# Optimization experiments

Measured on AMD Instinct MI355X. Metric: run time of the kernel, lower is better.

The kernel has to match this reference:

```python
import jax, jax.numpy as jnp
import numpy as np

N_NODES = 50000
NODE_DIM = 128
HIDDEN = 128
N_EDGES = 1600000
N_POSTS = 8192


def setup_inputs() -> dict:
    key = jax.random.key(0)
    ks = jax.random.split(key, 12)
    glorot = lambda k, shp: jax.random.normal(k, shp, jnp.float32) * (1.0 / np.sqrt(shp[0]))
    inp = {
        "node_features": jax.random.normal(ks[0], (N_NODES, NODE_DIM), jnp.float32),
        "edge_index": jax.random.randint(ks[1], (2, N_EDGES), 0, N_NODES, jnp.int32),
        "post_mask": jax.random.randint(ks[2], (N_POSTS,), 0, N_NODES, jnp.int32),
        # node_encoder: node_dim -> hidden
        "W_enc": glorot(ks[3], (NODE_DIM, HIDDEN)),
        "b_enc": jnp.zeros((HIDDEN,), jnp.float32),
        # conv1/conv2: hidden -> hidden
        "W1": glorot(ks[4], (HIDDEN, HIDDEN)),
        "b1": jnp.zeros((HIDDEN,), jnp.float32),
        "W2": glorot(ks[5], (HIDDEN, HIDDEN)),
        "b2": jnp.zeros((HIDDEN,), jnp.float32),
        # output head: hidden -> hidden//2 -> 1
        "W_o1": glorot(ks[6], (HIDDEN, HIDDEN // 2)),
        "b_o1": jnp.zeros((HIDDEN // 2,), jnp.float32),
        "W_o2": glorot(ks[7], (HIDDEN // 2, 1)),
        "b_o2": jnp.zeros((1,), jnp.float32),
    }
    return inp


def _aggregate(h, src, dst, n_nodes):
    # sum_{e: dst[e]=v} h[src[e]]  -- vectorized scatter-add (segment_sum)
    return jax.ops.segment_sum(h[src], dst, num_segments=n_nodes)


def reference(node_features, edge_index, post_mask,
              W_enc, b_enc, W1, b1, W2, b2, W_o1, b_o1, W_o2, b_o2):
    src, dst = edge_index[0], edge_index[1]
    n = node_features.shape[0]

    h = jax.nn.relu(node_features @ W_enc + b_enc)          # [N, H]
    agg = _aggregate(h, src, dst, n)                        # [N, H]
    h = jax.nn.relu((agg + h) @ W1 + b1)
    agg = _aggregate(h, src, dst, n)
    h = jax.nn.relu((agg + h) @ W2 + b2)

    post = h[post_mask]                                     # [P, H]
    hid = jax.nn.relu(post @ W_o1 + b_o1)                   # [P, H//2]
    logits = (hid @ W_o2 + b_o2).squeeze(-1)                # [P]
    return jax.nn.sigmoid(logits)
```

## Files before the change

kernel.cpp:

```cpp
#include <hip/hip_runtime.h>
#include <math.h>


typedef unsigned long long u64;

#define RB_SIZE   4096
#define RB_ROUNDS 16

__global__ __launch_bounds__(1024) void scan_part(const int* __restrict__ in,
                                                  int* __restrict__ bsum, int n) {
    __shared__ int red[1024];
    int i = blockIdx.x * 1024 + threadIdx.x;
    red[threadIdx.x] = (i < n) ? in[i] : 0;
    __syncthreads();
    for (int d = 512; d; d >>= 1) {
        if (threadIdx.x < d) red[threadIdx.x] += red[threadIdx.x + d];
        __syncthreads();
    }
    if (threadIdx.x == 0) bsum[blockIdx.x] = red[0];
}

__global__ __launch_bounds__(256) void scan_tops_par(const int* __restrict__ bsum,
                                                     int* __restrict__ bbase, int nb) {
    __shared__ int buf[256];
    int tid = threadIdx.x;
    int v = (tid < nb) ? bsum[tid] : 0;
    buf[tid] = v;
    __syncthreads();
    for (int s = 1; s < 256; s <<= 1) {
        int u = (tid >= s) ? buf[tid - s] : 0;
        __syncthreads();
        buf[tid] += u;
        __syncthreads();
    }
    if (tid < nb) bbase[tid] = buf[tid] - v;
}

__global__ __launch_bounds__(1024) void scan_final(const int* __restrict__ in,
                                                   const int* __restrict__ bbase,
                                                   int* __restrict__ out, int n) {
    __shared__ int buf[1024];
    int tid = threadIdx.x;
    int i = blockIdx.x * 1024 + tid;
    int c = (i < n) ? in[i] : 0;
    buf[tid] = c;
    __syncthreads();
    for (int d = 1; d < 1024; d <<= 1) {
        int v = (tid >= d) ? buf[tid - d] : 0;
        __syncthreads();
        buf[tid] += v;
        __syncthreads();
    }
    if (i < n) out[i] = bbase[blockIdx.x] + buf[tid] - c;
}

template <bool FIRST>
__global__ __launch_bounds__(256) void radix_hist(const int* __restrict__ dstArr,
                                                  const u64* __restrict__ recIn,
                                                  int* __restrict__ blockhist,
                                                  int E, int NBLK) {
    __shared__ int cnt[256];
    cnt[threadIdx.x] = 0;
    __syncthreads();
    int base = blockIdx.x * RB_SIZE;
    for (int t = threadIdx.x; t < RB_SIZE; t += 256) {
        int i = base + t;
        if (i < E) {
            int d = FIRST ? (dstArr[i] & 255)
                          : (int)((recIn[i] >> 8) & 255);
            atomicAdd(&cnt[d], 1);
        }
    }
    __syncthreads();
    blockhist[threadIdx.x * NBLK + blockIdx.x] = cnt[threadIdx.x];
}

template <bool FIRST>
__global__ __launch_bounds__(256) void radix_scatter(const int* __restrict__ dstArr,
                                                     const int* __restrict__ srcArr,
                                                     const u64* __restrict__ recIn,
                                                     u64* __restrict__ recOut,
                                                     int* __restrict__ csr_src,
                                                     int* __restrict__ csr_dst,
                                                     const int* __restrict__ blockbase,
                                                     int E, int NBLK) {
    __shared__ int cursor[256];
    __shared__ int gbase[256];
    __shared__ int cnt[256 * 4];
    __shared__ int wbase[256 * 4];
    int tid = threadIdx.x;
    int wid = tid >> 6, lane = tid & 63;
    cursor[tid] = 0;
    gbase[tid] = blockbase[tid * NBLK + blockIdx.x];
    int base = blockIdx.x * RB_SIZE;
    __syncthreads();
    for (int r = 0; r < RB_ROUNDS; ++r) {
        int i = base + r * 256 + tid;
        bool valid = (i < E);
        int d = 0;
        u64 rec = 0;
        if (valid) {
            if (FIRST) {
                int dv = dstArr[i];
                rec = ((u64)(unsigned)srcArr[i] << 32) | (unsigned)dv;
                d = dv & 255;
            } else {
                rec = recIn[i];
                d = (int)((rec >> 8) & 255);
            }
        }
        ((int4*)cnt)[tid] = make_int4(0, 0, 0, 0);
        u64 mask = ~0ull;
#pragma unroll
        for (int b = 0; b < 8; ++b) {
            int bit = (d >> b) & 1;
            u64 bal = __ballot(bit);
            mask &= bit ? bal : ~bal;
        }
        mask &= __ballot(valid ? 1 : 0);
        int rank = __popcll(mask & (((u64)1 << lane) - 1));
        int wtot = __popcll(mask);
        __syncthreads();
        if (valid && rank == 0) cnt[d * 4 + wid] = wtot;
        __syncthreads();
        {
            int run = cursor[tid];
#pragma unroll
            for (int w = 0; w < 4; ++w) {
                wbase[tid * 4 + w] = run;
                run += cnt[tid * 4 + w];
            }
            cursor[tid] = run;
        }
        __syncthreads();
        if (valid) {
            int pos = gbase[d] + wbase[d * 4 + wid] + rank;
            if (FIRST) {
                recOut[pos] = rec;
            } else {
                csr_src[pos] = (int)(rec >> 32);
                csr_dst[pos] = (int)(rec & 0xffffffffu);
            }
        }
        __syncthreads();
    }
}

__global__ __launch_bounds__(256) void boundary_kernel(const int* __restrict__ csr_dst,
                                                       int* __restrict__ offs,
                                                       int E, int N) {
    int e = blockIdx.x * 256 + threadIdx.x;
    if (e >= E) return;
    int cur = csr_dst[e];
    int prev = (e == 0) ? -1 : csr_dst[e - 1];
    for (int v = prev + 1; v <= cur; ++v) offs[v] = e;
    if (e == E - 1)
        for (int v = cur + 1; v <= N; ++v) offs[v] = E;
}

template <bool FUSE>
__global__ __launch_bounds__(256) void gemm128(const float* __restrict__ A,
                                               const float* __restrict__ A2,
                                               const float* __restrict__ W,
                                               const float* __restrict__ bias,
                                               float* __restrict__ out, int M) {
    __shared__ float Ws[64 * 128];
    __shared__ float As[32 * 128];
    int tid = threadIdx.x;
    int row0 = blockIdx.x * 32;

    float4* As4 = (float4*)As;
#pragma unroll
    for (int i = 0; i < 4; ++i) {
        int idx = tid + 256 * i;
        int r = idx >> 5, c = idx & 31;
        int gr = row0 + r;
        float4 v = make_float4(0.f, 0.f, 0.f, 0.f);
        if (gr < M) {
            v = ((const float4*)A)[gr * 32 + c];
            if (FUSE) {
                float4 u = ((const float4*)A2)[gr * 32 + c];
                v.x += u.x; v.y += u.y; v.z += u.z; v.w += u.w;
            }
        }
        As4[idx] = v;
    }

    int tx = tid & 31, ty = tid >> 5;
    float acc[4][4];
#pragma unroll
    for (int r = 0; r < 4; ++r)
#pragma unroll
        for (int c = 0; c < 4; ++c) acc[r][c] = 0.f;

    const float4* W4 = (const float4*)W;
    float4* Ws4 = (float4*)Ws;

    for (int kh = 0; kh < 2; ++kh) {
        __syncthreads();
#pragma unroll
        for (int i = 0; i < 8; ++i)
            Ws4[tid + 256 * i] = W4[kh * 2048 + tid + 256 * i];
        __syncthreads();

#pragma unroll 2
        for (int k = 0; k < 64; k += 4) {
            float4 a[4], b[4];
#pragma unroll
            for (int r = 0; r < 4; ++r)
                a[r] = *(const float4*)&As[(ty * 4 + r) * 128 + kh * 64 + k];
#pragma unroll
            for (int kk = 0; kk < 4; ++kk)
                b[kk] = *(const float4*)&Ws[(k + kk) * 128 + tx * 4];
#pragma unroll
            for (int r = 0; r < 4; ++r) {
                acc[r][0] = fmaf(a[r].x, b[0].x, acc[r][0]);
                acc[r][1] = fmaf(a[r].x, b[0].y, acc[r][1]);
                acc[r][2] = fmaf(a[r].x, b[0].z, acc[r][2]);
                acc[r][3] = fmaf(a[r].x, b[0].w, acc[r][3]);
                acc[r][0] = fmaf(a[r].y, b[1].x, acc[r][0]);
                acc[r][1] = fmaf(a[r].y, b[1].y, acc[r][1]);
                acc[r][2] = fmaf(a[r].y, b[1].z, acc[r][2]);
                acc[r][3] = fmaf(a[r].y, b[1].w, acc[r][3]);
                acc[r][0] = fmaf(a[r].z, b[2].x, acc[r][0]);
                acc[r][1] = fmaf(a[r].z, b[2].y, acc[r][1]);
                acc[r][2] = fmaf(a[r].z, b[2].z, acc[r][2]);
                acc[r][3] = fmaf(a[r].z, b[2].w, acc[r][3]);
                acc[r][0] = fmaf(a[r].w, b[3].x, acc[r][0]);
                acc[r][1] = fmaf(a[r].w, b[3].y, acc[r][1]);
                acc[r][2] = fmaf(a[r].w, b[3].z, acc[r][2]);
                acc[r][3] = fmaf(a[r].w, b[3].w, acc[r][3]);
            }
        }
    }

    float4 bv = *(const float4*)&bias[tx * 4];
#pragma unroll
    for (int r = 0; r < 4; ++r) {
        int gr = row0 + ty * 4 + r;
        if (gr < M) {
            float4 o;
            o.x = fmaxf(acc[r][0] + bv.x, 0.f);
            o.y = fmaxf(acc[r][1] + bv.y, 0.f);
            o.z = fmaxf(acc[r][2] + bv.z, 0.f);
            o.w = fmaxf(acc[r][3] + bv.w, 0.f);
            ((float4*)out)[gr * 32 + tx] = o;
        }
    }
}

__global__ __launch_bounds__(256) void aggregate_kernel(const float* __restrict__ h,
                                                        const int* __restrict__ offs,
                                                        const int* __restrict__ csr_src,
                                                        float* __restrict__ agg, int n) {
    int w = (blockIdx.x * 256 + threadIdx.x) >> 6;
    int lane = threadIdx.x & 63;
    int half = lane >> 5;
    int l32 = lane & 31;
    int node = w * 2 + half;
    bool nvalid = node < n;
    int beg = 0, deg = 0;
    if (nvalid) {
        beg = offs[node];
        deg = offs[node + 1] - beg;
    }
    int mdeg = max(deg, __shfl_xor(deg, 32));
    const float4* h4 = (const float4*)h;
    float ax = 0.f, ay = 0.f, az = 0.f, aw = 0.f;
    for (int base = 0; base < mdeg; base += 32) {
        int idx = base + l32;
        int sv = (nvalid && idx < deg) ? csr_src[beg + idx] : 0;
        int nk = mdeg - base; if (nk > 32) nk = 32;
#pragma unroll 4
        for (int j = 0; j < nk; ++j) {
            int s = __shfl(sv, (half << 5) | j);
            if (base + j < deg) {
                float4 r = h4[s * 32 + l32];
                ax += r.x; ay += r.y; az += r.z; aw += r.w;
            }
        }
    }
    if (nvalid) {
        float4 o = make_float4(ax, ay, az, aw);
        ((float4*)agg)[(size_t)node * 32 + l32] = o;
    }
}

__global__ __launch_bounds__(256) void head_kernel(const float* __restrict__ h,
                                                   const int* __restrict__ mask,
                                                   const float* __restrict__ Wo1,
                                                   const float* __restrict__ bo1,
                                                   const float* __restrict__ Wo2,
                                                   const float* __restrict__ bo2,
                                                   float* __restrict__ out, int P) {
    __shared__ float hids[4][64];
    int wid = threadIdx.x >> 6;
    int lane = threadIdx.x & 63;
    int p = blockIdx.x * 4 + wid;
    if (p >= P) return;
    int node = mask[p];
    const float* row = h + (size_t)node * 128;
    float acc = 0.f;
#pragma unroll 4
    for (int k = 0; k < 128; ++k)
        acc = fmaf(row[k], Wo1[k * 64 + lane], acc);
    hids[wid][lane] = fmaxf(acc + bo1[lane], 0.f);
    if (lane == 0) {
        double lg = 0.0;
        for (int j = 0; j < 64; ++j)
            lg = fma((double)hids[wid][j], (double)Wo2[j], lg);
        lg += (double)bo2[0];
        out[p] = (float)(1.0 / (1.0 + exp(-lg)));
    }
}

extern "C" void kernel_launch(void* const* d_in, const int* in_sizes, int n_in,
                              void* d_out, int out_size, void* d_ws, size_t ws_size,
                              hipStream_t stream) {
    const float* NF   = (const float*)d_in[0];
    const int*   EI   = (const int*)d_in[1];
    const int*   MASK = (const int*)d_in[2];
    const float* Wenc = (const float*)d_in[3];
    const float* benc = (const float*)d_in[4];
    const float* W1   = (const float*)d_in[5];
    const float* b1   = (const float*)d_in[6];
    const float* W2   = (const float*)d_in[7];
    const float* b2   = (const float*)d_in[8];
    const float* Wo1  = (const float*)d_in[9];
    const float* bo1  = (const float*)d_in[10];
    const float* Wo2  = (const float*)d_in[11];
    const float* bo2  = (const float*)d_in[12];
    float* out = (float*)d_out;

    const int N = in_sizes[0] / 128;
    const int E = in_sizes[1] / 2;
    const int P = in_sizes[2];

    char* ws = (char*)d_ws;
    size_t off = 0;
    auto alloc = [&](size_t bytes) {
        char* pp = ws + off;
        off += (bytes + 255) & ~(size_t)255;
        return pp;
    };
    float* h       = (float*)alloc((size_t)N * 128 * 4);
    float* agg     = (float*)alloc((size_t)N * 128 * 4);
    int*   offs    = (int*)alloc((size_t)(N + 1) * 4);
    int*   csr_src = (int*)alloc((size_t)E * 4);
    const int NBLK = (E + RB_SIZE - 1) / RB_SIZE;
    int*   bh      = (int*)alloc((size_t)256 * NBLK * 4);
    int*   bb      = (int*)alloc((size_t)256 * NBLK * 4);
    int*   bsum    = (int*)alloc(256 * 4);
    int*   bbase   = (int*)alloc(256 * 4);
    u64* rec_a   = (u64*)h;
    int* csr_dst = (int*)agg;

    const int* src = EI;
    const int* dst = EI + E;

    const int L = 256 * NBLK;
    const int nscanL = (L + 1023) / 1024;
    radix_hist<true><<<NBLK, 256, 0, stream>>>(dst, nullptr, bh, E, NBLK);
    scan_part<<<nscanL, 1024, 0, stream>>>(bh, bsum, L);
    scan_tops_par<<<1, 256, 0, stream>>>(bsum, bbase, nscanL);
    scan_final<<<nscanL, 1024, 0, stream>>>(bh, bbase, bb, L);
    radix_scatter<true><<<NBLK, 256, 0, stream>>>(dst, src, nullptr, rec_a,
                                                  nullptr, nullptr, bb, E, NBLK);
    radix_hist<false><<<NBLK, 256, 0, stream>>>(nullptr, rec_a, bh, E, NBLK);
    scan_part<<<nscanL, 1024, 0, stream>>>(bh, bsum, L);
    scan_tops_par<<<1, 256, 0, stream>>>(bsum, bbase, nscanL);
    scan_final<<<nscanL, 1024, 0, stream>>>(bh, bbase, bb, L);
    radix_scatter<false><<<NBLK, 256, 0, stream>>>(nullptr, nullptr, rec_a, nullptr,
                                                   csr_src, csr_dst, bb, E, NBLK);

    boundary_kernel<<<(E + 255) / 256, 256, 0, stream>>>(csr_dst, offs, E, N);

    int gblocks = (N + 31) / 32;
    int ablocks = ((N + 1) / 2 + 3) / 4;
    gemm128<false><<<gblocks, 256, 0, stream>>>(NF, nullptr, Wenc, benc, h, N);
    aggregate_kernel<<<ablocks, 256, 0, stream>>>(h, offs, csr_src, agg, N);
    gemm128<true><<<gblocks, 256, 0, stream>>>(h, agg, W1, b1, h, N);
    aggregate_kernel<<<ablocks, 256, 0, stream>>>(h, offs, csr_src, agg, N);
    gemm128<true><<<gblocks, 256, 0, stream>>>(h, agg, W2, b2, h, N);
    head_kernel<<<(P + 3) / 4, 256, 0, stream>>>(h, MASK, Wo1, bo1, Wo2, bo2, out, P);
}
```

Before: 412.4 us.

## Build CSR with one high-digit radix pass plus per-bucket LDS sort

Replaces the two-pass LSD radix sort and the separate boundary kernel with a single MSD scatter on dst>>8. It is followed by a bucket kernel that sorts each 256-node bucket by its low byte in shared memory and writes the CSR offsets directly. This removes one global histogram/scan/scatter pass over 1.6M 64-bit records, the csr_dst array and the boundary pass. In exchange each bucket is clamped to a fixed shared-memory capacity, so edges are silently dropped if a bucket ever exceeds it. The high-digit histogram also assumes at most 256 digits. With only about 196 bucket blocks, the kernel runs with low parallelism.

```diff
diff --git a/kernel.cpp b/kernel.cpp
--- a/kernel.cpp
+++ b/kernel.cpp
@@ -4,8 +4,9 @@
 
 typedef unsigned long long u64;
 
-#define RB_SIZE   4096
-#define RB_ROUNDS 16
+#define RB_SIZE    4096
+#define RB_ROUNDS  16
+#define BUCKET_CAP 9216
 
 __global__ __launch_bounds__(1024) void scan_part(const int* __restrict__ in,
                                                   int* __restrict__ bsum, int n) {
@@ -54,36 +55,26 @@
     if (i < n) out[i] = bbase[blockIdx.x] + buf[tid] - c;
 }
 
-template <bool FIRST>
-__global__ __launch_bounds__(256) void radix_hist(const int* __restrict__ dstArr,
-                                                  const u64* __restrict__ recIn,
-                                                  int* __restrict__ blockhist,
-                                                  int E, int NBLK) {
+__global__ __launch_bounds__(256) void radix_hist_hi(const int* __restrict__ dstArr,
+                                                     int* __restrict__ blockhist,
+                                                     int E, int NBLK) {
     __shared__ int cnt[256];
     cnt[threadIdx.x] = 0;
     __syncthreads();
     int base = blockIdx.x * RB_SIZE;
     for (int t = threadIdx.x; t < RB_SIZE; t += 256) {
         int i = base + t;
-        if (i < E) {
-            int d = FIRST ? (dstArr[i] & 255)
-                          : (int)((recIn[i] >> 8) & 255);
-            atomicAdd(&cnt[d], 1);
-        }
+        if (i < E) atomicAdd(&cnt[dstArr[i] >> 8], 1);
     }
     __syncthreads();
     blockhist[threadIdx.x * NBLK + blockIdx.x] = cnt[threadIdx.x];
 }
 
-template <bool FIRST>
-__global__ __launch_bounds__(256) void radix_scatter(const int* __restrict__ dstArr,
-                                                     const int* __restrict__ srcArr,
-                                                     const u64* __restrict__ recIn,
-                                                     u64* __restrict__ recOut,
-                                                     int* __restrict__ csr_src,
-                                                     int* __restrict__ csr_dst,
-                                                     const int* __restrict__ blockbase,
-                                                     int E, int NBLK) {
+__global__ __launch_bounds__(256) void radix_scatter_hi(const int* __restrict__ dstArr,
+                                                        const int* __restrict__ srcArr,
+                                                        u64* __restrict__ recOut,
+                                                        const int* __restrict__ blockbase,
+                                                        int E, int NBLK) {
     __shared__ int cursor[256];
     __shared__ int gbase[256];
     __shared__ int cnt[256 * 4];
@@ -100,14 +91,9 @@
         int d = 0;
         u64 rec = 0;
         if (valid) {
-            if (FIRST) {
-                int dv = dstArr[i];
-                rec = ((u64)(unsigned)srcArr[i] << 32) | (unsigned)dv;
-                d = dv & 255;
-            } else {
-                rec = recIn[i];
-                d = (int)((rec >> 8) & 255);
-            }
+            int dv = dstArr[i];
+            rec = ((u64)(unsigned)srcArr[i] << 32) | (unsigned)dv;
+            d = dv >> 8;
         }
         ((int4*)cnt)[tid] = make_int4(0, 0, 0, 0);
         u64 mask = ~0ull;
@@ -133,29 +119,88 @@
             cursor[tid] = run;
         }
         __syncthreads();
-        if (valid) {
-            int pos = gbase[d] + wbase[d * 4 + wid] + rank;
-            if (FIRST) {
-                recOut[pos] = rec;
-            } else {
-                csr_src[pos] = (int)(rec >> 32);
-                csr_dst[pos] = (int)(rec & 0xffffffffu);
+        if (valid) recOut[gbase[d] + wbase[d * 4 + wid] + rank] = rec;
+        __syncthreads();
+    }
+}
+
+__global__ __launch_bounds__(256) void bucket_kernel(const u64* __restrict__ rec,
+                                                     const int* __restrict__ blockbase,
+                                                     int* __restrict__ csr_src,
+                                                     int* __restrict__ offs,
+                                                     int E, int N, int NBLK, int NDIG) {
+    __shared__ int srcs[BUCKET_CAP];
+    __shared__ unsigned char lob[BUCKET_CAP];
+    __shared__ int binb[256];
+    __shared__ int cursor[256];
+    __shared__ int cnt4[256 * 4];
+    __shared__ int wbase4[256 * 4];
+    int g = blockIdx.x;
+    int tid = threadIdx.x;
+    int wid = tid >> 6, lane = tid & 63;
+    int gbeg = blockbase[g * NBLK];
+    int gend = (g + 1 < NDIG) ? blockbase[(g + 1) * NBLK] : E;
+    int cnt = gend - gbeg;
+    if (cnt > BUCKET_CAP) cnt = BUCKET_CAP;
+    binb[tid] = 0;
+    __syncthreads();
+    for (int i = tid; i < cnt; i += 256) {
+        u64 r = rec[gbeg + i];
+        srcs[i] = (int)(r >> 32);
+        int lo = (int)(r & 255);
+        lob[i] = (unsigned char)lo;
+        atomicAdd(&binb[lo], 1);
+    }
+    __syncthreads();
+    int c = binb[tid];
+    cursor[tid] = c;
+    __syncthreads();
+    for (int s = 1; s < 256; s <<= 1) {
+        int v = (tid >= s) ? cursor[tid - s] : 0;
+        __syncthreads();
+        cursor[tid] += v;
+        __syncthreads();
+    }
+    int excl = cursor[tid] - c;
+    __syncthreads();
+    binb[tid] = excl;
+    cursor[tid] = excl;
+    int v = g * 256 + tid;
+    if (v < N) offs[v] = gbeg + excl;
+    if (g == NDIG - 1 && tid == 0) offs[N] = E;
+    __syncthreads();
+    int nrounds = (cnt + 255) >> 8;
+    for (int r = 0; r < nrounds; ++r) {
+        int i = r * 256 + tid;
+        bool valid = (i < cnt);
+        int d = valid ? (int)lob[i] : 0;
+        ((int4*)cnt4)[tid] = make_int4(0, 0, 0, 0);
+        u64 mask = ~0ull;
+#pragma unroll
+        for (int b = 0; b < 8; ++b) {
+            int bit = (d >> b) & 1;
+            u64 bal = __ballot(bit);
+            mask &= bit ? bal : ~bal;
+        }
+        mask &= __ballot(valid ? 1 : 0);
+        int rank = __popcll(mask & (((u64)1 << lane) - 1));
+        int wtot = __popcll(mask);
+        __syncthreads();
+        if (valid && rank == 0) cnt4[d * 4 + wid] = wtot;
+        __syncthreads();
+        {
+            int run = cursor[tid];
+#pragma unroll
+            for (int w = 0; w < 4; ++w) {
+                wbase4[tid * 4 + w] = run;
+                run += cnt4[tid * 4 + w];
             }
-        }
-        __syncthreads();
-    }
-}
-
-__global__ __launch_bounds__(256) void boundary_kernel(const int* __restrict__ csr_dst,
-                                                       int* __restrict__ offs,
-                                                       int E, int N) {
-    int e = blockIdx.x * 256 + threadIdx.x;
-    if (e >= E) return;
-    int cur = csr_dst[e];
-    int prev = (e == 0) ? -1 : csr_dst[e - 1];
-    for (int v = prev + 1; v <= cur; ++v) offs[v] = e;
-    if (e == E - 1)
-        for (int v = cur + 1; v <= N; ++v) offs[v] = E;
+            cursor[tid] = run;
+        }
+        __syncthreads();
+        if (valid) csr_src[gbeg + wbase4[d * 4 + wid] + rank] = srcs[i];
+        __syncthreads();
+    }
 }
 
 template <bool FUSE>
@@ -352,28 +397,22 @@
     int*   bb      = (int*)alloc((size_t)256 * NBLK * 4);
     int*   bsum    = (int*)alloc(256 * 4);
     int*   bbase   = (int*)alloc(256 * 4);
-    u64* rec_a   = (u64*)h;
-    int* csr_dst = (int*)agg;
+    u64* rec_a = (u64*)h;
 
     const int* src = EI;
     const int* dst = EI + E;
 
-    const int L = 256 * NBLK;
+    const int NDIG = (N + 255) >> 8;
+    const int L = NDIG * NBLK;
     const int nscanL = (L + 1023) / 1024;
-    radix_hist<true><<<NBLK, 256, 0, stream>>>(dst, nullptr, bh, E, NBLK);
+
+    radix_hist_hi<<<NBLK, 256, 0, stream>>>(dst, bh, E, NBLK);
     scan_part<<<nscanL, 1024, 0, stream>>>(bh, bsum, L);
     scan_tops_par<<<1, 256, 0, stream>>>(bsum, bbase, nscanL);
     scan_final<<<nscanL, 1024, 0, stream>>>(bh, bbase, bb, L);
-    radix_scatter<true><<<NBLK, 256, 0, stream>>>(dst, src, nullptr, rec_a,
-                                                  nullptr, nullptr, bb, E, NBLK);
-    radix_hist<false><<<NBLK, 256, 0, stream>>>(nullptr, rec_a, bh, E, NBLK);
-    scan_part<<<nscanL, 1024, 0, stream>>>(bh, bsum, L);
-    scan_tops_par<<<1, 256, 0, stream>>>(bsum, bbase, nscanL);
-    scan_final<<<nscanL, 1024, 0, stream>>>(bh, bbase, bb, L);
-    radix_scatter<false><<<NBLK, 256, 0, stream>>>(nullptr, nullptr, rec_a, nullptr,
-                                                   csr_src, csr_dst, bb, E, NBLK);
-
-    boundary_kernel<<<(E + 255) / 256, 256, 0, stream>>>(csr_dst, offs, E, N);
+    radix_scatter_hi<<<NBLK, 256, 0, stream>>>(dst, src, rec_a, bb, E, NBLK);
+
+    bucket_kernel<<<NDIG, 256, 0, stream>>>(rec_a, bb, csr_src, offs, E, N, NBLK, NDIG);
 
     int gblocks = (N + 31) / 32;
     int ablocks = ((N + 1) / 2 + 3) / 4;
```

After: 397.3 us. 3.7% less time.
